# Kernel optimization log

Measured on AMD Instinct MI355X. Metric: run time of the kernel, lower is better.

Reference implementation:

```python
import jax, jax.numpy as jnp
import numpy as np

ALPHA = 1.0
ARAP_WEIGHT = 1.0
B, N, K, LATENT, HIDDEN = 16, 20000, 16, 256, 1024


def setup_inputs() -> dict:
    key = jax.random.key(0)
    ks = jax.random.split(key, 8)
    code = jax.random.normal(ks[0], (B, LATENT), jnp.float32)
    W1 = jax.random.normal(ks[1], (LATENT, HIDDEN), jnp.float32) / np.sqrt(LATENT)
    b1 = jnp.zeros((HIDDEN,), jnp.float32)
    W2 = jax.random.normal(ks[2], (HIDDEN, N * 3), jnp.float32) / np.sqrt(HIDDEN)
    b2 = jnp.zeros((N * 3,), jnp.float32)
    xyz1 = jax.random.normal(ks[3], (B, N, 3), jnp.float32)
    weightMatrix = jax.random.uniform(ks[4], (N, K), jnp.float32)
    area = jax.random.uniform(ks[5], (N,), jnp.float32)
    neighborsMatrix = jax.random.randint(ks[6], (N, K), 0, N, jnp.int32)
    numNeighbors = jax.random.randint(ks[7], (N,), 1, K + 1, jnp.int32)
    return {"code": code, "W1": W1, "b1": b1, "W2": W2, "b2": b2,
            "xyz1": xyz1, "weightMatrix": weightMatrix, "area": area,
            "neighborsMatrix": neighborsMatrix, "numNeighbors": numNeighbors}


def _mean_energy(code, W1, b1, W2, b2, xyz1, weightMatrix, area,
                 neighborsMatrix, numNeighbors):
    # decoder: MLP latent -> hidden -> N*3, reshaped to [B,N,3]
    h = jax.nn.relu(code @ W1 + b1)
    recon = (h @ W2 + b2).reshape(B, N, 3)

    # mask out padded neighbor slots, fold into weights  [N,K]
    mask = (jnp.arange(K)[None, :] < numNeighbors[:, None]).astype(jnp.float32)
    wm = weightMatrix * mask

    # neighbor-gathered edge vectors: rest pose d, deformed dq  [B,N,K,3]
    d = xyz1[:, :, None, :] - xyz1[:, neighborsMatrix, :]
    dq = recon[:, :, None, :] - recon[:, neighborsMatrix, :]

    # per-vertex weighted covariance and best-fit rotation (Procrustes)
    S = jnp.einsum('nk,bnki,bnkj->bnij', wm, d, dq)          # [B,N,3,3]
    U, s, Vt = jnp.linalg.svd(S)
    V = jnp.swapaxes(Vt, -1, -2)
    Ut = jnp.swapaxes(U, -1, -2)
    det = jnp.linalg.det(V @ Ut)                              # [B,N]
    Vf = V.at[..., :, -1].multiply(jnp.sign(det)[..., None])  # reflection fix
    R = jax.lax.stop_gradient(Vf @ Ut)                        # R treated as constant

    resid = dq - jnp.einsum('bnij,bnkj->bnki', R, d)          # [B,N,K,3]
    e = (ARAP_WEIGHT * ALPHA) * area[None, :, None] * wm[None] \
        * jnp.sum(resid * resid, axis=-1)                     # [B,N,K]
    # torch.mean(torch.mean(e, 2), 1)
    return jnp.mean(e, axis=(1, 2))                           # [B]


def reference(code, W1, b1, W2, b2, xyz1, weightMatrix, area,
              neighborsMatrix, numNeighbors):
    meanEnergy = _mean_energy(code, W1, b1, W2, b2, xyz1, weightMatrix, area,
                              neighborsMatrix, numNeighbors)
    # meanEnergy.backward(ones) -> grad of sum(meanEnergy) wrt code
    code_grad = jax.grad(lambda c: jnp.sum(
        _mean_energy(c, W1, b1, W2, b2, xyz1, weightMatrix, area,
                     neighborsMatrix, numNeighbors)))(code)
    return (meanEnergy, code_grad)
```

## Files before the change

### kernel.cpp

```cpp
#include <hip/hip_runtime.h>

constexpr int B_ = 16;
constexpr int NV = 20000;
constexpr int KN = 16;
constexpr int LAT = 256;
constexpr int HID = 1024;
constexpr int N3 = 60000;
constexpr int RCAP = 64;
constexpr int NCHUNK = 8;
constexpr float INV_NK = 1.0f / (20000.0f * 16.0f);

constexpr size_t H_OFF      = 0;
constexpr size_t XYZT_OFF   = H_OFF + B_ * HID;
constexpr size_t RECONT_OFF = XYZT_OFF + (size_t)N3 * 16;
constexpr size_t GRECON_OFF = RECONT_OFF + (size_t)N3 * 16;
constexpr size_t GH_OFF     = GRECON_OFF + (size_t)B_ * N3;
constexpr size_t OWNG_OFF   = GH_OFF + B_ * HID;
constexpr size_t GEDGE_OFF  = OWNG_OFF + (size_t)NV * 48;
constexpr size_t RCOUNT_OFF = GEDGE_OFF + (size_t)NV * KN * 48;
constexpr size_t RLIST_OFF  = RCOUNT_OFF + NV;
constexpr size_t PART_OFF   = RLIST_OFF + (size_t)NV * RCAP;

__device__ __forceinline__ void atomAddF(float* p, float v) {
  unsafeAtomicAdd(p, v);
}

__global__ __launch_bounds__(256) void k_mlp1(
    const float* __restrict__ code, const float* __restrict__ W1,
    const float* __restrict__ b1, float* __restrict__ h) {
  int t = blockIdx.x * 256 + threadIdx.x;
  int b = t >> 10, hd = t & 1023;
  const float* c = code + b * LAT;
  float acc = b1[hd];
  #pragma unroll 4
  for (int l = 0; l < LAT; ++l) acc += c[l] * W1[l * HID + hd];
  h[t] = fmaxf(acc, 0.0f);
}

__global__ __launch_bounds__(256) void k_xpose(
    const float* __restrict__ xyz, float* __restrict__ xyzT) {
  __shared__ float sm[64][17];
  const int tid = threadIdx.x;
  const int n30 = blockIdx.x * 64;
  {
    const int n3l = tid & 63, bq = tid >> 6;
    #pragma unroll
    for (int p = 0; p < 4; ++p) {
      int b = p * 4 + bq;
      if (n30 + n3l < N3) sm[n3l][b] = xyz[(size_t)b * N3 + n30 + n3l];
    }
  }
  __syncthreads();
  {
    const int b = tid & 15, nq = tid >> 4;
    #pragma unroll
    for (int p = 0; p < 4; ++p) {
      int n3l = p * 16 + nq;
      if (n30 + n3l < N3) xyzT[(size_t)(n30 + n3l) * 16 + b] = sm[n3l][b];
    }
  }
}

__global__ __launch_bounds__(256) void k_mlp2(
    const float* __restrict__ h, const float* __restrict__ W2,
    float* __restrict__ part) {
  __shared__ float hs[16][128];
  const int tid = threadIdx.x;
  const int hd0 = blockIdx.y * 128;
  #pragma unroll
  for (int r = 0; r < 8; ++r) {
    int idx = r * 256 + tid;
    int bb = idx >> 7, cc = idx & 127;
    hs[bb][cc] = h[bb * HID + hd0 + cc];
  }
  __syncthreads();

  const int j4 = blockIdx.x * 1024 + tid * 4;
  if (j4 >= N3) return;

  float4 acc[16];
  #pragma unroll
  for (int b = 0; b < 16; ++b) acc[b] = make_float4(0.f, 0.f, 0.f, 0.f);

  const float* wp = W2 + (size_t)hd0 * N3 + j4;
  float4 w0 = *(const float4*)(wp);
  float4 w1 = *(const float4*)(wp + (size_t)N3);
  float4 w2 = *(const float4*)(wp + (size_t)2 * N3);
  float4 w3 = *(const float4*)(wp + (size_t)3 * N3);

  for (int g = 0; g < 32; ++g) {
    const float* np = wp + (size_t)4 * N3;
    float4 n0, n1, n2, n3;
    if (g < 31) {
      n0 = *(const float4*)(np);
      n1 = *(const float4*)(np + (size_t)N3);
      n2 = *(const float4*)(np + (size_t)2 * N3);
      n3 = *(const float4*)(np + (size_t)3 * N3);
    }
    #pragma unroll
    for (int b = 0; b < 16; ++b) {
      float4 hb = *(const float4*)&hs[b][g * 4];
      acc[b].x += hb.x * w0.x + hb.y * w1.x + hb.z * w2.x + hb.w * w3.x;
      acc[b].y += hb.x * w0.y + hb.y * w1.y + hb.z * w2.y + hb.w * w3.y;
      acc[b].z += hb.x * w0.z + hb.y * w1.z + hb.z * w2.z + hb.w * w3.z;
      acc[b].w += hb.x * w0.w + hb.y * w1.w + hb.z * w2.w + hb.w * w3.w;
    }
    wp = np; w0 = n0; w1 = n1; w2 = n2; w3 = n3;
  }

  float ac[4][16];
  #pragma unroll
  for (int b = 0; b < 16; ++b) {
    ac[0][b] = acc[b].x; ac[1][b] = acc[b].y;
    ac[2][b] = acc[b].z; ac[3][b] = acc[b].w;
  }
  float* pbase = part + ((size_t)blockIdx.y * N3 + j4) * 16;
  #pragma unroll
  for (int jj = 0; jj < 4; ++jj)
    #pragma unroll
    for (int q = 0; q < 4; ++q)
      *(float4*)(pbase + jj * 16 + q * 4) = make_float4(
          ac[jj][q*4+0], ac[jj][q*4+1], ac[jj][q*4+2], ac[jj][q*4+3]);
}

__global__ __launch_bounds__(256) void k_reduce(
    const float* __restrict__ part, const float* __restrict__ b2,
    float* __restrict__ reconT) {
  int t = blockIdx.x * 256 + threadIdx.x;
  if (t >= N3 * 16 / 4) return;
  size_t pos = (size_t)t * 4;
  int j = t >> 2;
  float4 s = *(const float4*)(part + pos);
  #pragma unroll
  for (int c = 1; c < NCHUNK; ++c) {
    float4 p = *(const float4*)(part + (size_t)c * N3 * 16 + pos);
    s.x += p.x; s.y += p.y; s.z += p.z; s.w += p.w;
  }
  float bias = b2[j];
  s.x += bias; s.y += bias; s.z += bias; s.w += bias;
  *(float4*)(reconT + pos) = s;
}

__global__ __launch_bounds__(256) void k_fill(
    const int* __restrict__ nbrs, const int* __restrict__ nnbr,
    int* __restrict__ rcount, int* __restrict__ rlist) {
  int e = blockIdx.x * 256 + threadIdx.x;
  int n = e >> 4, k = e & 15;
  if (k < nnbr[n]) {
    int v = nbrs[e];
    int slot = atomicAdd(&rcount[v], 1);
    if (slot < RCAP) rlist[v * RCAP + slot] = e;
  }
}

__global__ __launch_bounds__(256, 2) void k_rot(
    const float* __restrict__ xT, const float* __restrict__ qT,
    const float* __restrict__ wmat, const float* __restrict__ area,
    const int* __restrict__ nbrs, const int* __restrict__ nnbr,
    float* __restrict__ ownG, float* __restrict__ gEdge,
    float* __restrict__ energy) {
  __shared__ float red[64];
  const int tid = threadIdx.x;
  const int b = tid & 15, nl = tid >> 4;
  const int n = blockIdx.x * 16 + nl;
  const int nn = nnbr[n];
  const float ar = area[n];
  const float x0 = xT[(size_t)n*48 + b],      x1 = xT[(size_t)n*48 + 16 + b],
              x2 = xT[(size_t)n*48 + 32 + b];
  const float q0 = qT[(size_t)n*48 + b],      q1 = qT[(size_t)n*48 + 16 + b],
              q2 = qT[(size_t)n*48 + 32 + b];

  float dX[KN], dY[KN], dZ[KN], eX[KN], eY[KN], eZ[KN], wk[KN];
  float S00=0,S01=0,S02=0,S10=0,S11=0,S12=0,S20=0,S21=0,S22=0;
  #pragma unroll
  for (int k = 0; k < KN; ++k) {
    float w=0, dx=0, dy=0, dz=0, ex=0, ey=0, ez=0;
    if (k < nn) {
      int m = nbrs[n * KN + k];
      w = wmat[n * KN + k];
      size_t mb = (size_t)m * 48 + b;
      dx = x0 - xT[mb]; dy = x1 - xT[mb + 16]; dz = x2 - xT[mb + 32];
      ex = q0 - qT[mb]; ey = q1 - qT[mb + 16]; ez = q2 - qT[mb + 32];
    }
    wk[k]=w; dX[k]=dx; dY[k]=dy; dZ[k]=dz; eX[k]=ex; eY[k]=ey; eZ[k]=ez;
    S00 += w*dx*ex; S01 += w*dx*ey; S02 += w*dx*ez;
    S10 += w*dy*ex; S11 += w*dy*ey; S12 += w*dy*ez;
    S20 += w*dz*ex; S21 += w*dz*ey; S22 += w*dz*ez;
  }

  float A00 = S00*S00 + S10*S10 + S20*S20;
  float A01 = S00*S01 + S10*S11 + S20*S21;
  float A02 = S00*S02 + S10*S12 + S20*S22;
  float A11 = S01*S01 + S11*S11 + S21*S21;
  float A12 = S01*S02 + S11*S12 + S21*S22;
  float A22 = S02*S02 + S12*S12 + S22*S22;
  float V00=1,V01=0,V02=0, V10=0,V11=1,V12=0, V20=0,V21=0,V22=1;

  auto rot = [&](float& app, float& aqq, float& apq, float& arp, float& arq,
                 float& vp0, float& vp1, float& vp2,
                 float& vq0, float& vq1, float& vq2) {
    float a = apq;
    if (fabsf(a) > 1e-37f) {
      float tau = (aqq - app) * 0.5f / a;
      float t = copysignf(1.0f, tau) / (fabsf(tau) + sqrtf(1.0f + tau * tau));
      float c = rsqrtf(1.0f + t * t);
      float s = t * c;
      float napp = c*c*app - 2.0f*s*c*a + s*s*aqq;
      float naqq = s*s*app + 2.0f*s*c*a + c*c*aqq;
      app = napp; aqq = naqq; apq = 0.0f;
      float rp = arp, rq = arq;
      arp = c*rp - s*rq; arq = s*rp + c*rq;
      float t0, t1;
      t0=vp0; t1=vq0; vp0 = c*t0 - s*t1; vq0 = s*t0 + c*t1;
      t0=vp1; t1=vq1; vp1 = c*t0 - s*t1; vq1 = s*t0 + c*t1;
      t0=vp2; t1=vq2; vp2 = c*t0 - s*t1; vq2 = s*t0 + c*t1;
    }
  };
  #pragma unroll
  for (int sweep = 0; sweep < 6; ++sweep) {
    rot(A00,A11,A01, A02,A12, V00,V10,V20, V01,V11,V21);
    rot(A00,A22,A02, A01,A12, V00,V10,V20, V02,V12,V22);
    rot(A11,A22,A12, A01,A02, V01,V11,V21, V02,V12,V22);
  }
  auto sw = [](float& a, float& c) { float t = a; a = c; c = t; };
  if (A00 < A11) { sw(A00,A11); sw(V00,V01); sw(V10,V11); sw(V20,V21); }
  if (A00 < A22) { sw(A00,A22); sw(V00,V02); sw(V10,V12); sw(V20,V22); }
  if (A11 < A22) { sw(A11,A22); sw(V01,V02); sw(V11,V12); sw(V21,V22); }

  float v1x=V00, v1y=V10, v1z=V20;
  float v2x=V01, v2y=V11, v2z=V21;

  float u1x = S00*v1x + S01*v1y + S02*v1z;
  float u1y = S10*v1x + S11*v1y + S12*v1z;
  float u1z = S20*v1x + S21*v1y + S22*v1z;
  float s1sq = u1x*u1x + u1y*u1y + u1z*u1z;
  if (s1sq > 1e-30f) { float r = rsqrtf(s1sq); u1x*=r; u1y*=r; u1z*=r; }
  else { u1x = 1.0f; u1y = 0.0f; u1z = 0.0f; }

  float u2x = S00*v2x + S01*v2y + S02*v2z;
  float u2y = S10*v2x + S11*v2y + S12*v2z;
  float u2z = S20*v2x + S21*v2y + S22*v2z;
  float pr = u2x*u1x + u2y*u1y + u2z*u1z;
  u2x -= pr*u1x; u2y -= pr*u1y; u2z -= pr*u1z;
  float s2sq = u2x*u2x + u2y*u2y + u2z*u2z;
  if (s2sq > 1e-12f * s1sq + 1e-30f) {
    float r = rsqrtf(s2sq); u2x*=r; u2y*=r; u2z*=r;
  } else {
    float ex_ = (fabsf(u1x) < 0.9f) ? 1.0f : 0.0f;
    float ey_ = 1.0f - ex_;
    float pp = ex_*u1x + ey_*u1y;
    u2x = ex_ - pp*u1x; u2y = ey_ - pp*u1y; u2z = -pp*u1z;
    float r = rsqrtf(u2x*u2x + u2y*u2y + u2z*u2z);
    u2x*=r; u2y*=r; u2z*=r;
  }
  float u3x = u1y*u2z - u1z*u2y, u3y = u1z*u2x - u1x*u2z, u3z = u1x*u2y - u1y*u2x;
  float v3x = v1y*v2z - v1z*v2y, v3y = v1z*v2x - v1x*v2z, v3z = v1x*v2y - v1y*v2x;

  float R00 = v1x*u1x + v2x*u2x + v3x*u3x;
  float R01 = v1x*u1y + v2x*u2y + v3x*u3y;
  float R02 = v1x*u1z + v2x*u2z + v3x*u3z;
  float R10 = v1y*u1x + v2y*u2x + v3y*u3x;
  float R11 = v1y*u1y + v2y*u2y + v3y*u3y;
  float R12 = v1y*u1z + v2y*u2z + v3y*u3z;
  float R20 = v1z*u1x + v2z*u2x + v3z*u3x;
  float R21 = v1z*u1y + v2z*u2y + v3z*u3y;
  float R22 = v1z*u1z + v2z*u2z + v3z*u3z;

  float esum = 0, go0 = 0, go1 = 0, go2 = 0;
  const float gf = 2.0f * ar * INV_NK;
  float* geb = gEdge + (size_t)n * 768 + b;
  #pragma unroll
  for (int k = 0; k < KN; ++k) {
    float w = wk[k];
    float dx = dX[k], dy = dY[k], dz = dZ[k];
    float rx = eX[k] - (R00*dx + R01*dy + R02*dz);
    float ry = eY[k] - (R10*dx + R11*dy + R12*dz);
    float rz = eZ[k] - (R20*dx + R21*dy + R22*dz);
    esum += w * (rx*rx + ry*ry + rz*rz);
    float gc = gf * w;
    float gx = gc*rx, gy = gc*ry, gz = gc*rz;
    go0 += gx; go1 += gy; go2 += gz;
    if (k < nn) {
      float* gp = geb + k * 48;
      gp[0] = gx; gp[16] = gy; gp[32] = gz;
    }
  }
  esum *= ar * INV_NK;

  float* og = ownG + (size_t)n * 48 + b;
  og[0] = go0; og[16] = go1; og[32] = go2;

  esum += __shfl_down(esum, 32);
  esum += __shfl_down(esum, 16);
  int wave = tid >> 6, lane = tid & 63;
  if (lane < 16) red[wave * 16 + lane] = esum;
  __syncthreads();
  if (tid < 16) atomAddF(&energy[tid], red[tid] + red[16 + tid] + red[32 + tid] + red[48 + tid]);
}

__global__ __launch_bounds__(256) void k_scatter(
    const float* __restrict__ gEdge, const float* __restrict__ ownG,
    const int* __restrict__ rcount, const int* __restrict__ rlist,
    float* __restrict__ grecon) {
  int t = blockIdx.x * 256 + threadIdx.x;
  int v = t >> 4, b = t & 15;
  const float* og = ownG + (size_t)v * 48 + b;
  float g0 = og[0], g1 = og[16], g2 = og[32];
  int deg = min(rcount[v], RCAP);
  const int* rl = rlist + v * RCAP;
  int i = 0;
  for (; i + 1 < deg; i += 2) {
    int e0 = rl[i], e1 = rl[i + 1];
    const float* p0 = gEdge + (size_t)e0 * 48 + b;
    const float* p1 = gEdge + (size_t)e1 * 48 + b;
    g0 -= p0[0]  + p1[0];
    g1 -= p0[16] + p1[16];
    g2 -= p0[32] + p1[32];
  }
  if (i < deg) {
    int e = rl[i];
    const float* p = gEdge + (size_t)e * 48 + b;
    g0 -= p[0]; g1 -= p[16]; g2 -= p[32];
  }
  float* gq = grecon + (size_t)b * N3 + v * 3;
  gq[0] = g0; gq[1] = g1; gq[2] = g2;
}

__global__ __launch_bounds__(256, 2) void k_mlp2_bwd(
    const float* __restrict__ gr, const float* __restrict__ W2,
    float* __restrict__ gh) {
  const int tid = threadIdx.x;
  const int lane = tid & 63;
  const int wv = tid >> 6;
  const int laneJ = lane & 15, laneR = lane >> 4;
  const int row0 = blockIdx.y * 32 + wv * 8 + laneR * 2;

  float4 acc0[16], acc1[16];
  #pragma unroll
  for (int b = 0; b < 16; ++b) {
    acc0[b] = make_float4(0.f, 0.f, 0.f, 0.f);
    acc1[b] = make_float4(0.f, 0.f, 0.f, 0.f);
  }

  const int jbase = blockIdx.x * 64 + laneJ * 4;
  const float* w2r0 = W2 + (size_t)row0 * N3;
  const float* w2r1 = W2 + (size_t)(row0 + 1) * N3;

  for (int it = 0; it < 59; ++it) {
    int j = jbase + it * 1024;
    if (j < N3) {
      float4 w0 = *(const float4*)(w2r0 + j);
      float4 w1 = *(const float4*)(w2r1 + j);
      #pragma unroll
      for (int b = 0; b < 16; ++b) {
        float4 g = *(const float4*)(gr + (size_t)b * N3 + j);
        acc0[b].x += g.x * w0.x; acc0[b].y += g.y * w0.y;
        acc0[b].z += g.z * w0.z; acc0[b].w += g.w * w0.w;
        acc1[b].x += g.x * w1.x; acc1[b].y += g.y * w1.y;
        acc1[b].z += g.z * w1.z; acc1[b].w += g.w * w1.w;
      }
    }
  }

  float s0[16], s1[16];
  #pragma unroll
  for (int b = 0; b < 16; ++b) {
    s0[b] = (acc0[b].x + acc0[b].y) + (acc0[b].z + acc0[b].w);
    s1[b] = (acc1[b].x + acc1[b].y) + (acc1[b].z + acc1[b].w);
  }
  #pragma unroll
  for (int m = 1; m <= 8; m <<= 1) {
    #pragma unroll
    for (int b = 0; b < 16; ++b) {
      s0[b] += __shfl_xor(s0[b], m);
      s1[b] += __shfl_xor(s1[b], m);
    }
  }
  if (laneJ == 0) {
    #pragma unroll
    for (int b = 0; b < 16; ++b) {
      atomAddF(&gh[b * HID + row0], s0[b]);
      atomAddF(&gh[b * HID + row0 + 1], s1[b]);
    }
  }
}

__global__ __launch_bounds__(256) void k_mlp1_bwd(
    const float* __restrict__ gh, const float* __restrict__ h,
    const float* __restrict__ W1, float* __restrict__ gcode) {
  __shared__ float gm[128];
  const int b = blockIdx.x;
  const int hd0 = blockIdx.y * 128;
  const int l = threadIdx.x;
  if (l < 128) {
    float g = gh[b * HID + hd0 + l];
    gm[l] = (h[b * HID + hd0 + l] > 0.0f) ? g : 0.0f;
  }
  __syncthreads();
  const float4* wp = (const float4*)(W1 + (size_t)l * HID + hd0);
  float acc = 0.0f;
  #pragma unroll
  for (int i = 0; i < 32; ++i) {
    float4 w4 = wp[i];
    acc += w4.x * gm[i*4+0] + w4.y * gm[i*4+1] + w4.z * gm[i*4+2] + w4.w * gm[i*4+3];
  }
  atomAddF(&gcode[b * LAT + l], acc);
}

extern "C" void kernel_launch(void* const* d_in, const int* in_sizes, int n_in,
                              void* d_out, int out_size, void* d_ws, size_t ws_size,
                              hipStream_t stream) {
  const float* code = (const float*)d_in[0];
  const float* W1   = (const float*)d_in[1];
  const float* b1   = (const float*)d_in[2];
  const float* W2   = (const float*)d_in[3];
  const float* b2   = (const float*)d_in[4];
  const float* xyz  = (const float*)d_in[5];
  const float* wmat = (const float*)d_in[6];
  const float* area = (const float*)d_in[7];
  const int* nbrs   = (const int*)d_in[8];
  const int* nnbr   = (const int*)d_in[9];

  float* out = (float*)d_out;
  float* ws = (float*)d_ws;
  float* h      = ws + H_OFF;
  float* xyzT   = ws + XYZT_OFF;
  float* reconT = ws + RECONT_OFF;
  float* grecon = ws + GRECON_OFF;
  float* gh     = ws + GH_OFF;
  float* ownG   = ws + OWNG_OFF;
  float* gEdge  = ws + GEDGE_OFF;
  int*   rcount = (int*)(ws + RCOUNT_OFF);
  int*   rlist  = (int*)(ws + RLIST_OFF);
  float* part   = ws + PART_OFF;

  hipMemsetAsync(gh, 0, (size_t)B_ * HID * sizeof(float), stream);
  hipMemsetAsync(rcount, 0, (size_t)NV * sizeof(int), stream);
  hipMemsetAsync(out, 0, (size_t)(B_ + B_ * LAT) * sizeof(float), stream);

  k_fill<<<dim3(NV * KN / 256), dim3(256), 0, stream>>>(nbrs, nnbr, rcount, rlist);
  k_xpose<<<dim3((N3 + 63) / 64), dim3(256), 0, stream>>>(xyz, xyzT);
  k_mlp1<<<dim3(64), dim3(256), 0, stream>>>(code, W1, b1, h);
  k_mlp2<<<dim3(59, NCHUNK), dim3(256), 0, stream>>>(h, W2, part);
  k_reduce<<<dim3((N3 * 16 / 4 + 255) / 256), dim3(256), 0, stream>>>(part, b2, reconT);
  k_rot<<<dim3(NV / 16), dim3(256), 0, stream>>>(
      xyzT, reconT, wmat, area, nbrs, nnbr, ownG, gEdge, out);
  k_scatter<<<dim3(NV * 16 / 256), dim3(256), 0, stream>>>(
      gEdge, ownG, rcount, rlist, grecon);
  k_mlp2_bwd<<<dim3(16, 32), dim3(256), 0, stream>>>(grecon, W2, gh);
  k_mlp1_bwd<<<dim3(B_, 8), dim3(256), 0, stream>>>(gh, h, W1, out + B_);
}
```

Measured before the change: 583.8 us.

## Merge prep kernels, interleave xyz/recon layout, float4 edge gradients, prefetch W2 in backward

Folds the three memsets, the transpose and the first MLP layer into one multi-role prep kernel, and merges the neighbor-list fill into the MLP2 launch as extra blocks. Rest and deformed positions are interleaved per vertex so k_rot gathers one contiguous 384-byte record per neighbor. Edge and own gradients are padded to float4 per batch lane so the scatter can use vector loads, unrolled by four. The MLP2 backward loop now software-prefetches the next W2 rows. This cuts launch overhead and uncoalesced gather traffic, but the padding adds a third more gradient storage and the fused kernels mix work of uneven cost.

Result: slower. 649.1 us (+11.2%).

```diff
diff --git a/kernel.cpp b/kernel.cpp
--- a/kernel.cpp
+++ b/kernel.cpp
@@ -11,13 +11,12 @@
 constexpr float INV_NK = 1.0f / (20000.0f * 16.0f);
 
 constexpr size_t H_OFF      = 0;
-constexpr size_t XYZT_OFF   = H_OFF + B_ * HID;
-constexpr size_t RECONT_OFF = XYZT_OFF + (size_t)N3 * 16;
-constexpr size_t GRECON_OFF = RECONT_OFF + (size_t)N3 * 16;
+constexpr size_t XQ_OFF     = H_OFF + B_ * HID;
+constexpr size_t GRECON_OFF = XQ_OFF + (size_t)NV * 96;
 constexpr size_t GH_OFF     = GRECON_OFF + (size_t)B_ * N3;
 constexpr size_t OWNG_OFF   = GH_OFF + B_ * HID;
-constexpr size_t GEDGE_OFF  = OWNG_OFF + (size_t)NV * 48;
-constexpr size_t RCOUNT_OFF = GEDGE_OFF + (size_t)NV * KN * 48;
+constexpr size_t GEDGE_OFF  = OWNG_OFF + (size_t)NV * 64;
+constexpr size_t RCOUNT_OFF = GEDGE_OFF + (size_t)NV * KN * 64;
 constexpr size_t RLIST_OFF  = RCOUNT_OFF + NV;
 constexpr size_t PART_OFF   = RLIST_OFF + (size_t)NV * RCAP;
 
@@ -25,48 +24,76 @@
   unsafeAtomicAdd(p, v);
 }
 
-__global__ __launch_bounds__(256) void k_mlp1(
-    const float* __restrict__ code, const float* __restrict__ W1,
-    const float* __restrict__ b1, float* __restrict__ h) {
-  int t = blockIdx.x * 256 + threadIdx.x;
-  int b = t >> 10, hd = t & 1023;
-  const float* c = code + b * LAT;
-  float acc = b1[hd];
-  #pragma unroll 4
-  for (int l = 0; l < LAT; ++l) acc += c[l] * W1[l * HID + hd];
-  h[t] = fmaxf(acc, 0.0f);
-}
-
-__global__ __launch_bounds__(256) void k_xpose(
-    const float* __restrict__ xyz, float* __restrict__ xyzT) {
-  __shared__ float sm[64][17];
+__global__ __launch_bounds__(256) void k_prep(
+    const float* __restrict__ xyz, const float* __restrict__ code,
+    const float* __restrict__ W1, const float* __restrict__ b1,
+    float* __restrict__ xq, float* __restrict__ h,
+    float* __restrict__ gh, float* __restrict__ out,
+    int* __restrict__ rcount) {
+  const int bid = blockIdx.x, tid = threadIdx.x;
+  if (bid < 938) {
+    __shared__ float sm[64][17];
+    const int n30 = bid * 64;
+    {
+      const int n3l = tid & 63, bq = tid >> 6;
+      #pragma unroll
+      for (int p = 0; p < 4; ++p) {
+        int b = p * 4 + bq;
+        if (n30 + n3l < N3) sm[n3l][b] = xyz[(size_t)b * N3 + n30 + n3l];
+      }
+    }
+    __syncthreads();
+    {
+      const int b = tid & 15, nq = tid >> 4;
+      #pragma unroll
+      for (int p = 0; p < 4; ++p) {
+        int n3 = n30 + p * 16 + nq;
+        if (n3 < N3) {
+          int n = n3 / 3, c = n3 - n * 3;
+          xq[(size_t)n * 96 + c * 16 + b] = sm[p * 16 + nq][b];
+        }
+      }
+    }
+  } else if (bid < 1002) {
+    int t = (bid - 938) * 256 + tid;
+    int b = t >> 10, hd = t & 1023;
+    const float* c = code + b * LAT;
+    float acc = b1[hd];
+    #pragma unroll 4
+    for (int l = 0; l < LAT; ++l) acc += c[l] * W1[l * HID + hd];
+    h[t] = fmaxf(acc, 0.0f);
+  } else if (bid < 1006) {
+    int base = (bid - 1002) * 4096 + tid;
+    #pragma unroll
+    for (int r = 0; r < 16; ++r) gh[base + r * 256] = 0.0f;
+  } else if (bid == 1006) {
+    for (int i = tid; i < B_ + B_ * LAT; i += 256) out[i] = 0.0f;
+  } else {
+    int i = (bid - 1007) * 256 + tid;
+    if (i < NV) rcount[i] = 0;
+  }
+}
+
+__global__ __launch_bounds__(256) void k_mlp2f(
+    const float* __restrict__ h, const float* __restrict__ W2,
+    float* __restrict__ part,
+    const int* __restrict__ nbrs, const int* __restrict__ nnbr,
+    int* __restrict__ rcount, int* __restrict__ rlist) {
+  const int bid = blockIdx.x;
   const int tid = threadIdx.x;
-  const int n30 = blockIdx.x * 64;
-  {
-    const int n3l = tid & 63, bq = tid >> 6;
-    #pragma unroll
-    for (int p = 0; p < 4; ++p) {
-      int b = p * 4 + bq;
-      if (n30 + n3l < N3) sm[n3l][b] = xyz[(size_t)b * N3 + n30 + n3l];
-    }
-  }
-  __syncthreads();
-  {
-    const int b = tid & 15, nq = tid >> 4;
-    #pragma unroll
-    for (int p = 0; p < 4; ++p) {
-      int n3l = p * 16 + nq;
-      if (n30 + n3l < N3) xyzT[(size_t)(n30 + n3l) * 16 + b] = sm[n3l][b];
-    }
-  }
-}
-
-__global__ __launch_bounds__(256) void k_mlp2(
-    const float* __restrict__ h, const float* __restrict__ W2,
-    float* __restrict__ part) {
+  if (bid >= 472) {
+    int e = (bid - 472) * 256 + tid;
+    int n = e >> 4, k = e & 15;
+    if (k < nnbr[n]) {
+      int v = nbrs[e];
+      int slot = atomicAdd(&rcount[v], 1);
+      if (slot < RCAP) rlist[v * RCAP + slot] = e;
+    }
+    return;
+  }
+  const int bx = bid % 59, by = bid / 59;
   __shared__ float hs[16][128];
-  const int tid = threadIdx.x;
-  const int hd0 = blockIdx.y * 128;
+  const int hd0 = by * 128;
   #pragma unroll
   for (int r = 0; r < 8; ++r) {
     int idx = r * 256 + tid;
@@ -75,7 +102,7 @@
   }
   __syncthreads();
 
-  const int j4 = blockIdx.x * 1024 + tid * 4;
+  const int j4 = bx * 1024 + tid * 4;
   if (j4 >= N3) return;
 
   float4 acc[16];
@@ -114,7 +141,7 @@
     ac[0][b] = acc[b].x; ac[1][b] = acc[b].y;
     ac[2][b] = acc[b].z; ac[3][b] = acc[b].w;
   }
-  float* pbase = part + ((size_t)blockIdx.y * N3 + j4) * 16;
+  float* pbase = part + ((size_t)by * N3 + j4) * 16;
   #pragma unroll
   for (int jj = 0; jj < 4; ++jj)
     #pragma unroll
@@ -125,11 +152,11 @@
 
 __global__ __launch_bounds__(256) void k_reduce(
     const float* __restrict__ part, const float* __restrict__ b2,
-    float* __restrict__ reconT) {
+    float* __restrict__ xq) {
   int t = blockIdx.x * 256 + threadIdx.x;
   if (t >= N3 * 16 / 4) return;
   size_t pos = (size_t)t * 4;
-  int j = t >> 2;
+  int j = t >> 2, bq = (t & 3) * 4;
   float4 s = *(const float4*)(part + pos);
   #pragma unroll
   for (int c = 1; c < NCHUNK; ++c) {
@@ -138,23 +165,12 @@
   }
   float bias = b2[j];
   s.x += bias; s.y += bias; s.z += bias; s.w += bias;
-  *(float4*)(reconT + pos) = s;
-}
-
-__global__ __launch_bounds__(256) void k_fill(
-    const int* __restrict__ nbrs, const int* __restrict__ nnbr,
-    int* __restrict__ rcount, int* __restrict__ rlist) {
-  int e = blockIdx.x * 256 + threadIdx.x;
-  int n = e >> 4, k = e & 15;
-  if (k < nnbr[n]) {
-    int v = nbrs[e];
-    int slot = atomicAdd(&rcount[v], 1);
-    if (slot < RCAP) rlist[v * RCAP + slot] = e;
-  }
+  int n = j / 3, c = j - n * 3;
+  *(float4*)(xq + (size_t)n * 96 + (3 + c) * 16 + bq) = s;
 }
 
 __global__ __launch_bounds__(256, 2) void k_rot(
-    const float* __restrict__ xT, const float* __restrict__ qT,
+    const float* __restrict__ xq,
     const float* __restrict__ wmat, const float* __restrict__ area,
     const int* __restrict__ nbrs, const int* __restrict__ nnbr,
     float* __restrict__ ownG, float* __restrict__ gEdge,
@@ -165,10 +181,9 @@
   const int n = blockIdx.x * 16 + nl;
   const int nn = nnbr[n];
   const float ar = area[n];
-  const float x0 = xT[(size_t)n*48 + b],      x1 = xT[(size_t)n*48 + 16 + b],
-              x2 = xT[(size_t)n*48 + 32 + b];
-  const float q0 = qT[(size_t)n*48 + b],      q1 = qT[(size_t)n*48 + 16 + b],
-              q2 = qT[(size_t)n*48 + 32 + b];
+  const float* xqn = xq + (size_t)n * 96 + b;
+  const float x0 = xqn[0],  x1 = xqn[16], x2 = xqn[32];
+  const float q0 = xqn[48], q1 = xqn[64], q2 = xqn[80];
 
   float dX[KN], dY[KN], dZ[KN], eX[KN], eY[KN], eZ[KN], wk[KN];
   float S00=0,S01=0,S02=0,S10=0,S11=0,S12=0,S20=0,S21=0,S22=0;
@@ -178,9 +193,9 @@
     if (k < nn) {
       int m = nbrs[n * KN + k];
       w = wmat[n * KN + k];
-      size_t mb = (size_t)m * 48 + b;
-      dx = x0 - xT[mb]; dy = x1 - xT[mb + 16]; dz = x2 - xT[mb + 32];
-      ex = q0 - qT[mb]; ey = q1 - qT[mb + 16]; ez = q2 - qT[mb + 32];
+      const float* mp = xq + (size_t)m * 96 + b;
+      dx = x0 - mp[0];  dy = x1 - mp[16]; dz = x2 - mp[32];
+      ex = q0 - mp[48]; ey = q1 - mp[64]; ez = q2 - mp[80];
     }
     wk[k]=w; dX[k]=dx; dY[k]=dy; dZ[k]=dz; eX[k]=ex; eY[k]=ey; eZ[k]=ez;
     S00 += w*dx*ex; S01 += w*dx*ey; S02 += w*dx*ez;
@@ -268,7 +283,7 @@
 
   float esum = 0, go0 = 0, go1 = 0, go2 = 0;
   const float gf = 2.0f * ar * INV_NK;
-  float* geb = gEdge + (size_t)n * 768 + b;
+  float* geb = gEdge + (size_t)n * 1024 + b * 4;
   #pragma unroll
   for (int k = 0; k < KN; ++k) {
     float w = wk[k];
@@ -281,14 +296,12 @@
     float gx = gc*rx, gy = gc*ry, gz = gc*rz;
     go0 += gx; go1 += gy; go2 += gz;
     if (k < nn) {
-      float* gp = geb + k * 48;
-      gp[0] = gx; gp[16] = gy; gp[32] = gz;
+      *(float4*)(geb + k * 64) = make_float4(gx, gy, gz, 0.0f);
     }
   }
   esum *= ar * INV_NK;
 
-  float* og = ownG + (size_t)n * 48 + b;
-  og[0] = go0; og[16] = go1; og[32] = go2;
+  *(float4*)(ownG + (size_t)n * 64 + b * 4) = make_float4(go0, go1, go2, 0.0f);
 
   esum += __shfl_down(esum, 32);
   esum += __shfl_down(esum, 16);
@@ -304,23 +317,25 @@
     float* __restrict__ grecon) {
   int t = blockIdx.x * 256 + threadIdx.x;
   int v = t >> 4, b = t & 15;
-  const float* og = ownG + (size_t)v * 48 + b;
-  float g0 = og[0], g1 = og[16], g2 = og[32];
+  const float4 og = *(const float4*)(ownG + (size_t)v * 64 + b * 4);
+  float g0 = og.x, g1 = og.y, g2 = og.z;
   int deg = min(rcount[v], RCAP);
   const int* rl = rlist + v * RCAP;
   int i = 0;
-  for (; i + 1 < deg; i += 2) {
-    int e0 = rl[i], e1 = rl[i + 1];
-    const float* p0 = gEdge + (size_t)e0 * 48 + b;
-    const float* p1 = gEdge + (size_t)e1 * 48 + b;
-    g0 -= p0[0]  + p1[0];
-    g1 -= p0[16] + p1[16];
-    g2 -= p0[32] + p1[32];
-  }
-  if (i < deg) {
+  for (; i + 3 < deg; i += 4) {
+    int e0 = rl[i], e1 = rl[i + 1], e2 = rl[i + 2], e3 = rl[i + 3];
+    float4 p0 = *(const float4*)(gEdge + (size_t)e0 * 64 + b * 4);
+    float4 p1 = *(const float4*)(gEdge + (size_t)e1 * 64 + b * 4);
+    float4 p2 = *(const float4*)(gEdge + (size_t)e2 * 64 + b * 4);
+    float4 p3 = *(const float4*)(gEdge + (size_t)e3 * 64 + b * 4);
+    g0 -= (p0.x + p1.x) + (p2.x + p3.x);
+    g1 -= (p0.y + p1.y) + (p2.y + p3.y);
+    g2 -= (p0.z + p1.z) + (p2.z + p3.z);
+  }
+  for (; i < deg; ++i) {
     int e = rl[i];
-    const float* p = gEdge + (size_t)e * 48 + b;
-    g0 -= p[0]; g1 -= p[16]; g2 -= p[32];
+    float4 p = *(const float4*)(gEdge + (size_t)e * 64 + b * 4);
+    g0 -= p.x; g1 -= p.y; g2 -= p.z;
   }
   float* gq = grecon + (size_t)b * N3 + v * 3;
   gq[0] = g0; gq[1] = g1; gq[2] = g2;
@@ -344,21 +359,37 @@
 
   const int jbase = blockIdx.x * 64 + laneJ * 4;
   const float* w2r0 = W2 + (size_t)row0 * N3;
-  const float* w2r1 = W2 + (size_t)(row0 + 1) * N3;
-
-  for (int it = 0; it < 59; ++it) {
-    int j = jbase + it * 1024;
-    if (j < N3) {
-      float4 w0 = *(const float4*)(w2r0 + j);
-      float4 w1 = *(const float4*)(w2r1 + j);
-      #pragma unroll
-      for (int b = 0; b < 16; ++b) {
-        float4 g = *(const float4*)(gr + (size_t)b * N3 + j);
-        acc0[b].x += g.x * w0.x; acc0[b].y += g.y * w0.y;
-        acc0[b].z += g.z * w0.z; acc0[b].w += g.w * w0.w;
-        acc1[b].x += g.x * w1.x; acc1[b].y += g.y * w1.y;
-        acc1[b].z += g.z * w1.z; acc1[b].w += g.w * w1.w;
-      }
+  const float* w2r1 = w2r0 + N3;
+
+  int j = jbase;
+  float4 w0 = *(const float4*)(w2r0 + j);
+  float4 w1 = *(const float4*)(w2r1 + j);
+  #pragma unroll 2
+  for (int it = 0; it < 58; ++it) {
+    int jn = j + 1024;
+    float4 nw0, nw1;
+    if (jn < N3) {
+      nw0 = *(const float4*)(w2r0 + jn);
+      nw1 = *(const float4*)(w2r1 + jn);
+    }
+    #pragma unroll
+    for (int b = 0; b < 16; ++b) {
+      float4 g = *(const float4*)(gr + (size_t)b * N3 + j);
+      acc0[b].x += g.x * w0.x; acc0[b].y += g.y * w0.y;
+      acc0[b].z += g.z * w0.z; acc0[b].w += g.w * w0.w;
+      acc1[b].x += g.x * w1.x; acc1[b].y += g.y * w1.y;
+      acc1[b].z += g.z * w1.z; acc1[b].w += g.w * w1.w;
+    }
+    j = jn; w0 = nw0; w1 = nw1;
+  }
+  if (j < N3) {
+    #pragma unroll
+    for (int b = 0; b < 16; ++b) {
+      float4 g = *(const float4*)(gr + (size_t)b * N3 + j);
+      acc0[b].x += g.x * w0.x; acc0[b].y += g.y * w0.y;
+      acc0[b].z += g.z * w0.z; acc0[b].w += g.w * w0.w;
+      acc1[b].x += g.x * w1.x; acc1[b].y += g.y * w1.y;
+      acc1[b].z += g.z * w1.z; acc1[b].w += g.w * w1.w;
     }
   }
 
@@ -424,8 +455,7 @@
   float* out = (float*)d_out;
   float* ws = (float*)d_ws;
   float* h      = ws + H_OFF;
-  float* xyzT   = ws + XYZT_OFF;
-  float* reconT = ws + RECONT_OFF;
+  float* xq     = ws + XQ_OFF;
   float* grecon = ws + GRECON_OFF;
   float* gh     = ws + GH_OFF;
   float* ownG   = ws + OWNG_OFF;
@@ -434,17 +464,12 @@
   int*   rlist  = (int*)(ws + RLIST_OFF);
   float* part   = ws + PART_OFF;
 
-  hipMemsetAsync(gh, 0, (size_t)B_ * HID * sizeof(float), stream);
-  hipMemsetAsync(rcount, 0, (size_t)NV * sizeof(int), stream);
-  hipMemsetAsync(out, 0, (size_t)(B_ + B_ * LAT) * sizeof(float), stream);
-
-  k_fill<<<dim3(NV * KN / 256), dim3(256), 0, stream>>>(nbrs, nnbr, rcount, rlist);
-  k_xpose<<<dim3((N3 + 63) / 64), dim3(256), 0, stream>>>(xyz, xyzT);
-  k_mlp1<<<dim3(64), dim3(256), 0, stream>>>(code, W1, b1, h);
-  k_mlp2<<<dim3(59, NCHUNK), dim3(256), 0, stream>>>(h, W2, part);
-  k_reduce<<<dim3((N3 * 16 / 4 + 255) / 256), dim3(256), 0, stream>>>(part, b2, reconT);
+  k_prep<<<dim3(1086), dim3(256), 0, stream>>>(xyz, code, W1, b1, xq, h, gh, out, rcount);
+  k_mlp2f<<<dim3(472 + NV * KN / 256), dim3(256), 0, stream>>>(
+      h, W2, part, nbrs, nnbr, rcount, rlist);
+  k_reduce<<<dim3((N3 * 16 / 4 + 255) / 256), dim3(256), 0, stream>>>(part, b2, xq);
   k_rot<<<dim3(NV / 16), dim3(256), 0, stream>>>(
-      xyzT, reconT, wmat, area, nbrs, nnbr, ownG, gEdge, out);
+      xq, wmat, area, nbrs, nnbr, ownG, gEdge, out);
   k_scatter<<<dim3(NV * 16 / 256), dim3(256), 0, stream>>>(
       gEdge, ownG, rcount, rlist, grecon);
   k_mlp2_bwd<<<dim3(16, 32), dim3(256), 0, stream>>>(grecon, W2, gh);
```
